# Performance work log

Hardware: AMD Instinct MI355X
Metric: run time of the kernel (lower is better)

The kernel has to match this reference:

```python
import jax, jax.numpy as jnp
import numpy as np

MAX_DIST = 35.0
GRID_RES = 1.0
BOX = int(np.ceil(2 * MAX_DIST / GRID_RES + 1))  # 71


def setup_inputs() -> dict:
    key = jax.random.key(0)
    k1, k2 = jax.random.split(key)
    B, N, F = 8, 16384, 32
    # spread ~N(0, 20): most points inside [-35, 35] box, some outside (mask path)
    coords = jax.random.normal(k1, (B, N, 3), dtype=jnp.float32) * 20.0
    features = jax.random.normal(k2, (B, N, F), dtype=jnp.float32)
    return {"coords": coords, "features": features}


def reference(coords, features):
    B, N, _ = coords.shape
    F = features.shape[2]
    # quantize coords to integer grid cells
    gc = jnp.round((coords + MAX_DIST) / GRID_RES).astype(jnp.int32)  # [B,N,3]
    in_box = jnp.all((gc >= 0) & (gc < BOX), axis=2)                  # [B,N]
    # jit-friendly equivalent of boolean_mask+scatter_nd: zero out-of-box
    # updates and clamp their indices (adding zero is a no-op).
    gc_c = jnp.clip(gc, 0, BOX - 1)
    upd = jnp.where(in_box[..., None], features, 0.0)                 # [B,N,F]
    grid = jnp.zeros((B, BOX, BOX, BOX, F), dtype=features.dtype)
    # FAITHFUL to original: batch index column is tf.zeros -> every point
    # scatters (with duplicate-index summation) into batch slice 0.
    grid = grid.at[0, gc_c[..., 0], gc_c[..., 1], gc_c[..., 2]].add(upd)
    return grid
```

## Files before the change

### kernel.cpp

```cpp
#include <hip/hip_runtime.h>

#define BOX 71
#define NF 32
#define MAX_DIST_F 35.0f

__global__ __launch_bounds__(256) void MakeGrid_zero_kernel(
    float4* __restrict__ out, size_t n4)
{
    size_t stride = (size_t)gridDim.x * blockDim.x;
    for (size_t i = (size_t)blockIdx.x * blockDim.x + threadIdx.x; i < n4; i += stride) {
        out[i] = make_float4(0.f, 0.f, 0.f, 0.f);
    }
}

__global__ __launch_bounds__(256) void MakeGrid_scatter_kernel(
    const float* __restrict__ coords,
    const float* __restrict__ features,
    float* __restrict__ grid,
    int total_points)
{
    int t = blockIdx.x * blockDim.x + threadIdx.x;
    int p = t >> 5;
    int f = t & 31;
    if (p >= total_points) return;

    float cx = coords[p * 3 + 0];
    float cy = coords[p * 3 + 1];
    float cz = coords[p * 3 + 2];

    int gx = (int)rintf(cx + MAX_DIST_F);
    int gy = (int)rintf(cy + MAX_DIST_F);
    int gz = (int)rintf(cz + MAX_DIST_F);

    bool in_box = (gx >= 0) & (gx < BOX) &
                  (gy >= 0) & (gy < BOX) &
                  (gz >= 0) & (gz < BOX);
    if (!in_box) return;

    float v = features[(size_t)p * NF + f];
    size_t idx = (((size_t)gx * BOX + gy) * BOX + gz) * NF + f;
    atomicAdd(grid + idx, v);
}

extern "C" void kernel_launch(void* const* d_in, const int* in_sizes, int n_in,
                              void* d_out, int out_size, void* d_ws, size_t ws_size,
                              hipStream_t stream) {
    const float* coords   = (const float*)d_in[0];
    const float* features = (const float*)d_in[1];
    float* out = (float*)d_out;

    size_t n4 = (size_t)out_size / 4;
    MakeGrid_zero_kernel<<<8192, 256, 0, stream>>>((float4*)out, n4);

    int total_points = in_sizes[0] / 3;
    int total_threads = total_points * NF;
    int blocks = (total_threads + 255) / 256;
    MakeGrid_scatter_kernel<<<blocks, 256, 0, stream>>>(coords, features, out, total_points);
}
```

Measured before the change: 381.0 us.

## Zero only slice 0 first, overlap remaining zeroing with scatter in fused kernel

Only batch slice 0, the one that receives the scatter atomics, is zeroed before the scatter. The other seven slices are zeroed with nontemporal stores inside the scatter kernel. Blocks are partitioned so one in four runs a grid-stride scatter loop and the other three zero the rest of the output. This lets the bandwidth-bound zero fill overlap with the atomic scatter, at the cost of fewer blocks working on the scatter.

```diff
diff --git a/kernel.cpp b/kernel.cpp
--- a/kernel.cpp
+++ b/kernel.cpp
@@ -3,43 +3,62 @@
 #define BOX 71
 #define NF 32
 #define MAX_DIST_F 35.0f
+#define SLICE_FLOATS (BOX * BOX * BOX * NF)
 
-__global__ __launch_bounds__(256) void MakeGrid_zero_kernel(
-    float4* __restrict__ out, size_t n4)
+typedef float vfloat4 __attribute__((ext_vector_type(4)));
+
+__global__ __launch_bounds__(256) void MakeGrid_zero_slice0(
+    vfloat4* __restrict__ out, int n4)
 {
-    size_t stride = (size_t)gridDim.x * blockDim.x;
-    for (size_t i = (size_t)blockIdx.x * blockDim.x + threadIdx.x; i < n4; i += stride) {
-        out[i] = make_float4(0.f, 0.f, 0.f, 0.f);
-    }
+    int stride = gridDim.x * blockDim.x;
+    vfloat4 z = {0.f, 0.f, 0.f, 0.f};
+    for (int i = blockIdx.x * blockDim.x + threadIdx.x; i < n4; i += stride)
+        out[i] = z;
 }
 
-__global__ __launch_bounds__(256) void MakeGrid_scatter_kernel(
+__global__ __launch_bounds__(256) void MakeGrid_fused_scatter_zero(
     const float* __restrict__ coords,
     const float* __restrict__ features,
     float* __restrict__ grid,
-    int total_points)
+    vfloat4* __restrict__ rest,
+    size_t rest_n4,
+    int total_tasks)
 {
-    int t = blockIdx.x * blockDim.x + threadIdx.x;
-    int p = t >> 5;
-    int f = t & 31;
-    if (p >= total_points) return;
+    int b = blockIdx.x;
+    int tid = threadIdx.x;
 
-    float cx = coords[p * 3 + 0];
-    float cy = coords[p * 3 + 1];
-    float cz = coords[p * 3 + 2];
+    if ((b & 3) == 0) {
+        int sb = b >> 2;
+        int stride = (gridDim.x >> 2) * blockDim.x;
+        for (int t = sb * blockDim.x + tid; t < total_tasks; t += stride) {
+            int p = t >> 5;
+            int f = t & 31;
 
-    int gx = (int)rintf(cx + MAX_DIST_F);
-    int gy = (int)rintf(cy + MAX_DIST_F);
-    int gz = (int)rintf(cz + MAX_DIST_F);
+            float cx = coords[p * 3 + 0];
+            float cy = coords[p * 3 + 1];
+            float cz = coords[p * 3 + 2];
 
-    bool in_box = (gx >= 0) & (gx < BOX) &
-                  (gy >= 0) & (gy < BOX) &
-                  (gz >= 0) & (gz < BOX);
-    if (!in_box) return;
+            int gx = (int)rintf(cx + MAX_DIST_F);
+            int gy = (int)rintf(cy + MAX_DIST_F);
+            int gz = (int)rintf(cz + MAX_DIST_F);
 
-    float v = features[(size_t)p * NF + f];
-    size_t idx = (((size_t)gx * BOX + gy) * BOX + gz) * NF + f;
-    atomicAdd(grid + idx, v);
+            bool in_box = (gx >= 0) & (gx < BOX) &
+                          (gy >= 0) & (gy < BOX) &
+                          (gz >= 0) & (gz < BOX);
+            if (!in_box) continue;
+
+            float v = features[(size_t)p * NF + f];
+            size_t idx = (((size_t)gx * BOX + gy) * BOX + gz) * NF + f;
+            atomicAdd(grid + idx, v);
+        }
+    } else {
+        size_t zb = (size_t)(b >> 2) * 3 + (size_t)(b & 3) - 1;
+        size_t nzb = ((size_t)gridDim.x >> 2) * 3;
+        size_t stride = nzb * blockDim.x;
+        vfloat4 z = {0.f, 0.f, 0.f, 0.f};
+        for (size_t i = zb * blockDim.x + tid; i < rest_n4; i += stride)
+            __builtin_nontemporal_store(z, &rest[i]);
+    }
 }
 
 extern "C" void kernel_launch(void* const* d_in, const int* in_sizes, int n_in,
@@ -49,11 +68,15 @@
     const float* features = (const float*)d_in[1];
     float* out = (float*)d_out;
 
-    size_t n4 = (size_t)out_size / 4;
-    MakeGrid_zero_kernel<<<8192, 256, 0, stream>>>((float4*)out, n4);
+    int total_points = in_sizes[0] / 3;
+    int total_tasks = total_points * NF;
 
-    int total_points = in_sizes[0] / 3;
-    int total_threads = total_points * NF;
-    int blocks = (total_threads + 255) / 256;
-    MakeGrid_scatter_kernel<<<blocks, 256, 0, stream>>>(coords, features, out, total_points);
+    int slice0_n4 = SLICE_FLOATS / 4;
+    MakeGrid_zero_slice0<<<4096, 256, 0, stream>>>((vfloat4*)out, slice0_n4);
+
+    size_t rest_n4 = ((size_t)out_size - SLICE_FLOATS) / 4;
+    vfloat4* rest = (vfloat4*)(out + SLICE_FLOATS);
+
+    MakeGrid_fused_scatter_zero<<<8192, 256, 0, stream>>>(
+        coords, features, out, rest, rest_n4, total_tasks);
 }
```

Result: no change. 388.1 us (+1.9%).
